# Performance work log

Hardware: AMD Instinct MI355X
Metric: run time of the kernel (lower is better)

The kernel has to match this reference:

```python
import jax, jax.numpy as jnp
import numpy as np

IN_F = 4096
OUT_F = 11008
GROUP_SIZE = 128
NUM_GROUPS = (IN_F + GROUP_SIZE - 1) // GROUP_SIZE  # 32
N_HIGH = int(OUT_F * 0.25)   # 2752
N_LOW = OUT_F - N_HIGH       # 8256
B, S = 2, 2048


def setup_inputs() -> dict:
    key = jax.random.key(0)
    ks = jax.random.split(key, 9)
    x = jax.random.normal(ks[0], (B, S, IN_F), dtype=jnp.float32)
    # INT8 symmetric codes for high-precision columns
    high_prec_weight = jax.random.randint(ks[1], (IN_F, N_HIGH), -128, 128, dtype=jnp.int32)
    # per-group, per-column scales (positive, realistic magnitude)
    high_prec_scales = jax.random.uniform(ks[2], (NUM_GROUPS, N_HIGH), jnp.float32, 1e-4, 2e-2)
    # 4-bit asymmetric codes in [0, 15]
    low_prec_weight = jax.random.randint(ks[3], (IN_F, N_LOW), 0, 16, dtype=jnp.int32)
    low_prec_scales = jax.random.uniform(ks[4], (IN_F, 1), jnp.float32, 1e-4, 2e-2)
    low_prec_scales2 = jax.random.uniform(ks[5], (1, N_LOW), jnp.float32, 0.5, 2.0)
    low_prec_zeros = jnp.round(jax.random.uniform(ks[6], (IN_F, 1), jnp.float32, 0.0, 15.0))
    # inverse column permutation restoring original order
    col_indices_inv = jax.random.permutation(ks[7], OUT_F).astype(jnp.int64)
    bias = jax.random.normal(ks[8], (OUT_F,), dtype=jnp.float32) * 0.02
    return {
        "x": x,
        "high_prec_weight": high_prec_weight,
        "high_prec_scales": high_prec_scales,
        "low_prec_weight": low_prec_weight,
        "low_prec_scales": low_prec_scales,
        "low_prec_scales2": low_prec_scales2,
        "low_prec_zeros": low_prec_zeros,
        "col_indices_inv": col_indices_inv,
        "bias": bias,
    }


def _dequantize(high_w, high_scales, low_w, low_s1, low_s2, low_z, col_inv):
    # High: group-wise symmetric INT8 dequant. K divisible by GROUP_SIZE here (no pad).
    w_high = (high_w.astype(jnp.float32)
              .reshape(NUM_GROUPS, GROUP_SIZE, N_HIGH)
              * high_scales[:, None, :]).reshape(IN_F, N_HIGH)
    # Low: SINQ dual-scale asymmetric dequant: ((q - z) * s1) * s2
    w_low = (low_w.astype(jnp.float32) - low_z) * low_s1 * low_s2
    # Reassemble original column order: W_kn [in_features, out_features]
    w = jnp.concatenate([w_high, w_low], axis=1)[:, col_inv]
    return w


def reference(x, high_prec_weight, high_prec_scales, low_prec_weight,
              low_prec_scales, low_prec_scales2, low_prec_zeros,
              col_indices_inv, bias):
    w_kn = _dequantize(high_prec_weight, high_prec_scales, low_prec_weight,
                       low_prec_scales, low_prec_scales2, low_prec_zeros,
                       col_indices_inv)
    # F.linear(x, W_original) with W_original = w_kn.T  ->  x @ w_kn
    out = jnp.einsum('bsk,kn->bsn', x, w_kn) + bias
    return out
```

## Files before the change

### kernel.cpp

```cpp
#include <hip/hip_runtime.h>
#include <hip/hip_bf16.h>

#define IN_F   4096
#define OUT_F  11008
#define NHIGH  2752
#define NLOW   8256
#define M_TOT  4096

typedef __attribute__((ext_vector_type(8))) short bf16x8;
typedef __attribute__((ext_vector_type(4))) float f32x4;
typedef __attribute__((ext_vector_type(4))) float f32x4v;

__device__ __forceinline__ short f2bf(float f) {
    union { float f; unsigned u; } v; v.f = f;
    unsigned r = (v.u + 0x7fffu + ((v.u >> 16) & 1u)) >> 16;
    return (short)(r & 0xffffu);
}

__device__ __forceinline__ void async16(const void* g, const void* l) {
    __builtin_amdgcn_global_load_lds(
        (const __attribute__((address_space(1))) unsigned int*)g,
        (__attribute__((address_space(3))) unsigned int*)l, 16, 0, 0);
}

__global__ void fwd_perm_kernel(const int* __restrict__ cinv, int* __restrict__ fwd) {
    int n = blockIdx.x * blockDim.x + threadIdx.x;
    if (n < OUT_F) fwd[cinv[n]] = n;
}

__global__ void cvt_x_kernel(const float* __restrict__ x, short* __restrict__ xb) {
    const int nv = (M_TOT * IN_F) / 8;
    for (int i = blockIdx.x * blockDim.x + threadIdx.x; i < nv;
         i += gridDim.x * blockDim.x) {
        const f32x4v* p = (const f32x4v*)(x + (long)i * 8);
        f32x4v a = __builtin_nontemporal_load(p);
        f32x4v b = __builtin_nontemporal_load(p + 1);
        bf16x8 o;
        o[0] = f2bf(a[0]); o[1] = f2bf(a[1]); o[2] = f2bf(a[2]); o[3] = f2bf(a[3]);
        o[4] = f2bf(b[0]); o[5] = f2bf(b[1]); o[6] = f2bf(b[2]); o[7] = f2bf(b[3]);
        *(bf16x8*)(xb + (long)i * 8) = o;
    }
}

__global__ void dequant_kernel(const int* __restrict__ hw, const float* __restrict__ hs,
                               const int* __restrict__ lw, const float* __restrict__ s1,
                               const float* __restrict__ s2, const float* __restrict__ zp,
                               const int* __restrict__ fwd,
                               short* __restrict__ wt) {
    __shared__ short tile[64 * 66];
    const int t  = threadIdx.x;
    const int c0 = blockIdx.x * 64;
    const int k0 = blockIdx.y * 64;
    const int cl = t & 63;
    const int w  = t >> 6;

    if (c0 < NHIGH) {
        const int ci = c0 + cl;
        #pragma unroll
        for (int i = 0; i < 16; ++i) {
            const int kl = w + 4 * i;
            const int k  = k0 + kl;
            int   q   = __builtin_nontemporal_load(&hw[(long)k * NHIGH + ci]);
            float val = (float)q * hs[(k >> 7) * NHIGH + ci];
            tile[cl * 66 + kl] = f2bf(val);
        }
    } else {
        const int ci = c0 - NHIGH + cl;
        const float s2v = s2[ci];
        #pragma unroll
        for (int i = 0; i < 16; ++i) {
            const int kl = w + 4 * i;
            const int k  = k0 + kl;
            int   q   = __builtin_nontemporal_load(&lw[(long)k * NLOW + ci]);
            float val = ((float)q - zp[k]) * s1[k] * s2v;
            tile[cl * 66 + kl] = f2bf(val);
        }
    }
    __syncthreads();
    const int oc = t >> 2;
    const int kq = (t & 3) * 16;
    bf16x8 o0, o1;
    #pragma unroll
    for (int j = 0; j < 8; ++j) {
        o0[j] = tile[oc * 66 + kq + j];
        o1[j] = tile[oc * 66 + kq + 8 + j];
    }
    const int ndst = fwd[c0 + oc];
    short* dst = wt + (long)ndst * IN_F + k0 + kq;
    *(bf16x8*)dst       = o0;
    *(bf16x8*)(dst + 8) = o1;
}

#define BM 256
#define BN 256
#define BK 64
#define KT (IN_F / BK)
#define NTIL (OUT_F / BN)
#define MTIL (M_TOT / BM)
#define NWG2 (NTIL * MTIL)

#define BAR()    __builtin_amdgcn_s_barrier()
#define LGKM0()  asm volatile("s_waitcnt lgkmcnt(0)" ::: "memory")
#define VMC(N)   asm volatile("s_waitcnt vmcnt(" #N ")" ::: "memory")

__global__ __launch_bounds__(512, 2) void gemm_kernel(
    const short* __restrict__ A,
    const short* __restrict__ Bt,
    const float* __restrict__ bias,
    float* __restrict__ C) {
    __shared__ __align__(16) short lds_s[65536];
    char* const lds = (char*)lds_s;

    const int t    = threadIdx.x;
    const int lane = t & 63;
    const int w    = t >> 6;
    const int wr   = w >> 2;
    const int wc   = w & 3;

    const int swz = (blockIdx.x % 8) * (NWG2 / 8) + blockIdx.x / 8;
    const int nb  = swz / MTIL;
    const int mb  = swz % MTIL;
    const int m0  = mb * BM;
    const int n0  = nb * BN;

    const int srow = w * 8 + (lane >> 3);
    const int scb  = ((lane & 7) ^ (lane >> 3)) * 16;
    const char* gA0 = (const char*)A  + (long)(m0 + srow) * (IN_F * 2) + scb;
    const char* gB0 = (const char*)Bt + (long)(n0 + srow) * (IN_F * 2) + scb;

    const int rl  = (lane & 15) * 128;
    const int kb0 = ((lane >> 4) * 16) ^ ((lane & 7) << 4);
    const int kb1 = kb0 ^ 64;

#define STAGE(gbase, region_off, h, ktile) do {                                  \
        const char* _g = (gbase) + (long)((h) * 128) * (IN_F * 2) + (ktile) * 128; \
        char* _l = lds + (region_off) + (h) * 16384 + w * 1024;                  \
        async16(_g,                      _l);                                    \
        async16(_g + (long)64 * (IN_F * 2), _l + 8192);                          \
    } while (0)

    f32x4 acc[8][4];
    #pragma unroll
    for (int i = 0; i < 8; ++i)
        #pragma unroll
        for (int j = 0; j < 4; ++j)
            acc[i][j] = (f32x4){0.f, 0.f, 0.f, 0.f};

    bf16x8 a[4][2], b0[2][2], b1[2][2];

#define RD_A(buf, mq) do {                                                       \
        char* _p = lds + (buf) * 65536 + wr * 16384 + (mq) * 8192 + rl;          \
        _Pragma("unroll")                                                        \
        for (int _j = 0; _j < 4; ++_j) {                                         \
            a[_j][0] = *(const bf16x8*)(_p + _j * 2048 + kb0);                   \
            a[_j][1] = *(const bf16x8*)(_p + _j * 2048 + kb1);                   \
        }                                                                        \
    } while (0)

#define RD_B(buf, nq, breg) do {                                                 \
        char* _p = lds + (buf) * 65536 + 32768 + wc * 8192 + (nq) * 4096 + rl;   \
        _Pragma("unroll")                                                        \
        for (int _n = 0; _n < 2; ++_n) {                                         \
            breg[_n][0] = *(const bf16x8*)(_p + _n * 2048 + kb0);                \
            breg[_n][1] = *(const bf16x8*)(_p + _n * 2048 + kb1);                \
        }                                                                        \
    } while (0)

#define MMA_Q(mq, nq, breg) do {                                                 \
        __builtin_amdgcn_s_setprio(1);                                           \
        _Pragma("unroll")                                                        \
        for (int _j = 0; _j < 4; ++_j)                                           \
        _Pragma("unroll")                                                        \
        for (int _n = 0; _n < 2; ++_n) {                                         \
            acc[(mq)*4+_j][(nq)*2+_n] = __builtin_amdgcn_mfma_f32_16x16x32_bf16( \
                a[_j][0], breg[_n][0], acc[(mq)*4+_j][(nq)*2+_n], 0, 0, 0);      \
            acc[(mq)*4+_j][(nq)*2+_n] = __builtin_amdgcn_mfma_f32_16x16x32_bf16( \
                a[_j][1], breg[_n][1], acc[(mq)*4+_j][(nq)*2+_n], 0, 0, 0);      \
        }                                                                        \
        __builtin_amdgcn_s_setprio(0);                                           \
    } while (0)

    STAGE(gA0, 0,     0, 0);
    STAGE(gA0, 0,     1, 0);
    STAGE(gB0, 32768, 0, 0);
    STAGE(gB0, 32768, 1, 0);
    STAGE(gA0, 65536, 0, 1);
    VMC(2);
    BAR();

    #pragma unroll 1
    for (int it = 0; it < KT / 2; ++it) {
        const int kt1 = 2 * it + 1;
        const int kt2 = (2 * it + 2 < KT) ? 2 * it + 2 : KT - 1;
        const int kt3 = (2 * it + 3 < KT) ? 2 * it + 3 : KT - 1;

        RD_A(0, 0); RD_B(0, 0, b0);
        STAGE(gA0, 65536 + 0,     1, kt1);
        BAR(); LGKM0();
        MMA_Q(0, 0, b0);
        BAR();

        RD_B(0, 1, b1);
        STAGE(gB0, 65536 + 32768, 0, kt1);
        BAR(); LGKM0();
        MMA_Q(0, 1, b1);
        BAR();

        RD_A(0, 1);
        STAGE(gB0, 65536 + 32768, 1, kt1);
        BAR(); LGKM0();
        MMA_Q(1, 1, b1);
        BAR();

        STAGE(gA0, 0,             0, kt2);
        BAR();
        MMA_Q(1, 0, b0);
        VMC(2);
        BAR();

        RD_A(1, 0); RD_B(1, 0, b0);
        STAGE(gA0, 0,             1, kt2);
        BAR(); LGKM0();
        MMA_Q(0, 0, b0);
        BAR();

        RD_B(1, 1, b1);
        STAGE(gB0, 32768,         0, kt2);
        BAR(); LGKM0();
        MMA_Q(0, 1, b1);
        BAR();

        RD_A(1, 1);
        STAGE(gB0, 32768,         1, kt2);
        BAR(); LGKM0();
        MMA_Q(1, 1, b1);
        BAR();

        STAGE(gA0, 65536,         0, kt3);
        BAR();
        MMA_Q(1, 0, b0);
        VMC(2);
        BAR();
    }

    asm volatile("s_waitcnt vmcnt(0)" ::: "memory");

    const int er = m0 + wr * 128 + (lane >> 4) * 4;
    const int ec = n0 + wc * 64 + (lane & 15);
    #pragma unroll
    for (int ni = 0; ni < 4; ++ni) {
        const float bv = bias[ec + ni * 16];
        #pragma unroll
        for (int mi = 0; mi < 8; ++mi) {
            #pragma unroll
            for (int r = 0; r < 4; ++r) {
                __builtin_nontemporal_store(
                    acc[mi][ni][r] + bv,
                    &C[(long)(er + mi * 16 + r) * OUT_F + ec + ni * 16]);
            }
        }
    }
}

extern "C" void kernel_launch(void* const* d_in, const int* in_sizes, int n_in,
                              void* d_out, int out_size, void* d_ws, size_t ws_size,
                              hipStream_t stream) {
    const float* x    = (const float*)d_in[0];
    const int*   hw   = (const int*)d_in[1];
    const float* hs   = (const float*)d_in[2];
    const int*   lw   = (const int*)d_in[3];
    const float* s1   = (const float*)d_in[4];
    const float* s2   = (const float*)d_in[5];
    const float* zp   = (const float*)d_in[6];
    const int*   cinv = (const int*)d_in[7];
    const float* bias = (const float*)d_in[8];
    float*       out  = (float*)d_out;

    short* wt  = (short*)d_ws;
    short* xb  = (short*)((char*)d_ws + (size_t)OUT_F * IN_F * 2);
    int*   fwd = (int*)((char*)d_ws + (size_t)OUT_F * IN_F * 2
                                    + (size_t)M_TOT * IN_F * 2);

    fwd_perm_kernel<<<(OUT_F + 255) / 256, 256, 0, stream>>>(cinv, fwd);
    cvt_x_kernel<<<2048, 256, 0, stream>>>(x, xb);
    dequant_kernel<<<dim3(OUT_F / 64, IN_F / 64), 256, 0, stream>>>(
        hw, hs, lw, s1, s2, zp, fwd, wt);
    gemm_kernel<<<NWG2, 512, 0, stream>>>(xb, wt, bias, out);
}
```

Measured before the change: 404.7 us.

## Deepen async prefetch pipeline, remap wave quadrants, and use grouped tile swizzle

Changes the block-to-tile mapping so that groups of four M tiles share an N tile, aiming for better L2 reuse of B. Remaps each wave's sub-tile so a quadrant is interleaved across waves rather than contiguous. Reorders the global→LDS staging so more loads stay in flight (vmcnt 8 instead of 2), adding a wait after each MMA phase. The deeper prefetch is meant to hide memory latency, at the cost of more complex ordering and a risk of LDS hazards if the wait counts are wrong.

Measured after the change: 400.3 us. Within noise of the previous version (-1.1%).

```diff
diff --git a/kernel.cpp b/kernel.cpp
--- a/kernel.cpp
+++ b/kernel.cpp
@@ -117,11 +117,13 @@
     const int wr   = w >> 2;
     const int wc   = w & 3;
 
-    const int swz = (blockIdx.x % 8) * (NWG2 / 8) + blockIdx.x / 8;
-    const int nb  = swz / MTIL;
-    const int mb  = swz % MTIL;
-    const int m0  = mb * BM;
-    const int n0  = nb * BN;
+    const int swz   = (blockIdx.x % 8) * (NWG2 / 8) + blockIdx.x / 8;
+    const int sr    = swz / (4 * NTIL);
+    const int in_sr = swz % (4 * NTIL);
+    const int nb    = in_sr / 4;
+    const int mb    = sr * 4 + (in_sr & 3);
+    const int m0    = mb * BM;
+    const int n0    = nb * BN;
 
     const int srow = w * 8 + (lane >> 3);
     const int scb  = ((lane & 7) ^ (lane >> 3)) * 16;
@@ -135,7 +137,7 @@
 #define STAGE(gbase, region_off, h, ktile) do {                                  \
         const char* _g = (gbase) + (long)((h) * 128) * (IN_F * 2) + (ktile) * 128; \
         char* _l = lds + (region_off) + (h) * 16384 + w * 1024;                  \
-        async16(_g,                      _l);                                    \
+        async16(_g,                        _l);                                  \
         async16(_g + (long)64 * (IN_F * 2), _l + 8192);                          \
     } while (0)
 
@@ -148,8 +150,8 @@
 
     bf16x8 a[4][2], b0[2][2], b1[2][2];
 
-#define RD_A(buf, mq) do {                                                       \
-        char* _p = lds + (buf) * 65536 + wr * 16384 + (mq) * 8192 + rl;          \
+#define RD_A(buf, qm) do {                                                       \
+        char* _p = lds + (buf) * 65536 + (qm) * 16384 + wr * 8192 + rl;          \
         _Pragma("unroll")                                                        \
         for (int _j = 0; _j < 4; ++_j) {                                         \
             a[_j][0] = *(const bf16x8*)(_p + _j * 2048 + kb0);                   \
@@ -157,8 +159,8 @@
         }                                                                        \
     } while (0)
 
-#define RD_B(buf, nq, breg) do {                                                 \
-        char* _p = lds + (buf) * 65536 + 32768 + wc * 8192 + (nq) * 4096 + rl;   \
+#define RD_B(buf, qn, breg) do {                                                 \
+        char* _p = lds + (buf) * 65536 + 32768 + (qn) * 16384 + wc * 4096 + rl;  \
         _Pragma("unroll")                                                        \
         for (int _n = 0; _n < 2; ++_n) {                                         \
             breg[_n][0] = *(const bf16x8*)(_p + _n * 2048 + kb0);                \
@@ -166,97 +168,91 @@
         }                                                                        \
     } while (0)
 
-#define MMA_Q(mq, nq, breg) do {                                                 \
+#define MMA_Q(qm, qn, breg) do {                                                 \
         __builtin_amdgcn_s_setprio(1);                                           \
         _Pragma("unroll")                                                        \
         for (int _j = 0; _j < 4; ++_j)                                           \
         _Pragma("unroll")                                                        \
         for (int _n = 0; _n < 2; ++_n) {                                         \
-            acc[(mq)*4+_j][(nq)*2+_n] = __builtin_amdgcn_mfma_f32_16x16x32_bf16( \
-                a[_j][0], breg[_n][0], acc[(mq)*4+_j][(nq)*2+_n], 0, 0, 0);      \
-            acc[(mq)*4+_j][(nq)*2+_n] = __builtin_amdgcn_mfma_f32_16x16x32_bf16( \
-                a[_j][1], breg[_n][1], acc[(mq)*4+_j][(nq)*2+_n], 0, 0, 0);      \
+            acc[(qm)*4+_j][(qn)*2+_n] = __builtin_amdgcn_mfma_f32_16x16x32_bf16( \
+                a[_j][0], breg[_n][0], acc[(qm)*4+_j][(qn)*2+_n], 0, 0, 0);      \
+            acc[(qm)*4+_j][(qn)*2+_n] = __builtin_amdgcn_mfma_f32_16x16x32_bf16( \
+                a[_j][1], breg[_n][1], acc[(qm)*4+_j][(qn)*2+_n], 0, 0, 0);      \
         }                                                                        \
         __builtin_amdgcn_s_setprio(0);                                           \
     } while (0)
 
-    STAGE(gA0, 0,     0, 0);
-    STAGE(gA0, 0,     1, 0);
-    STAGE(gB0, 32768, 0, 0);
-    STAGE(gB0, 32768, 1, 0);
-    STAGE(gA0, 65536, 0, 1);
-    VMC(2);
+    STAGE(gA0, 0,             0, 0);
+    STAGE(gB0, 32768,         0, 0);
+    STAGE(gB0, 32768,         1, 0);
+    STAGE(gA0, 0,             1, 0);
+    STAGE(gA0, 65536,         0, 1);
+    STAGE(gB0, 65536 + 32768, 0, 1);
+    VMC(8);
     BAR();
 
     #pragma unroll 1
     for (int it = 0; it < KT / 2; ++it) {
         const int kt1 = 2 * it + 1;
-        const int kt2 = (2 * it + 2 < KT) ? 2 * it + 2 : KT - 1;
-        const int kt3 = (2 * it + 3 < KT) ? 2 * it + 3 : KT - 1;
+        const int c2  = (2 * it + 2 < KT) ? 2 * it + 2 : KT - 1;
+        const int c3  = (2 * it + 3 < KT) ? 2 * it + 3 : KT - 1;
+        const int r2  = (c2 & 1) * 65536;
+        const int r3  = (c3 & 1) * 65536;
 
         RD_A(0, 0); RD_B(0, 0, b0);
-        STAGE(gA0, 65536 + 0,     1, kt1);
+        STAGE(gB0, 65536 + 32768, 1, kt1);
         BAR(); LGKM0();
         MMA_Q(0, 0, b0);
-        BAR();
-
+        VMC(8); BAR();
         RD_B(0, 1, b1);
-        STAGE(gB0, 65536 + 32768, 0, kt1);
+        STAGE(gA0, 65536,         1, kt1);
         BAR(); LGKM0();
         MMA_Q(0, 1, b1);
-        BAR();
-
+        VMC(8); BAR();
         RD_A(0, 1);
-        STAGE(gB0, 65536 + 32768, 1, kt1);
+        STAGE(gA0, r2,            0, c2);
         BAR(); LGKM0();
         MMA_Q(1, 1, b1);
         BAR();
-
-        STAGE(gA0, 0,             0, kt2);
+        STAGE(gB0, r2 + 32768,    0, c2);
         BAR();
         MMA_Q(1, 0, b0);
-        VMC(2);
-        BAR();
+        VMC(8); BAR();
 
         RD_A(1, 0); RD_B(1, 0, b0);
-        STAGE(gA0, 0,             1, kt2);
+        STAGE(gB0, r2 + 32768,    1, c2);
         BAR(); LGKM0();
         MMA_Q(0, 0, b0);
-        BAR();
-
+        VMC(8); BAR();
         RD_B(1, 1, b1);
-        STAGE(gB0, 32768,         0, kt2);
+        STAGE(gA0, r2,            1, c2);
         BAR(); LGKM0();
         MMA_Q(0, 1, b1);
-        BAR();
-
+        VMC(8); BAR();
         RD_A(1, 1);
-        STAGE(gB0, 32768,         1, kt2);
+        STAGE(gA0, r3,            0, c3);
         BAR(); LGKM0();
         MMA_Q(1, 1, b1);
         BAR();
-
-        STAGE(gA0, 65536,         0, kt3);
+        STAGE(gB0, r3 + 32768,    0, c3);
         BAR();
         MMA_Q(1, 0, b0);
-        VMC(2);
-        BAR();
+        VMC(8); BAR();
     }
 
     asm volatile("s_waitcnt vmcnt(0)" ::: "memory");
 
-    const int er = m0 + wr * 128 + (lane >> 4) * 4;
-    const int ec = n0 + wc * 64 + (lane & 15);
     #pragma unroll
     for (int ni = 0; ni < 4; ++ni) {
-        const float bv = bias[ec + ni * 16];
+        const int ec = n0 + (ni >> 1) * 128 + wc * 32 + (ni & 1) * 16 + (lane & 15);
+        const float bv = bias[ec];
         #pragma unroll
         for (int mi = 0; mi < 8; ++mi) {
+            const int er = m0 + (mi >> 2) * 128 + wr * 64 + (mi & 3) * 16 + (lane >> 4) * 4;
             #pragma unroll
             for (int r = 0; r < 4; ++r) {
-                __builtin_nontemporal_store(
-                    acc[mi][ni][r] + bv,
-                    &C[(long)(er + mi * 16 + r) * OUT_F + ec + ni * 16]);
+                __builtin_nontemporal_store(acc[mi][ni][r] + bv,
+                                            &C[(long)(er + r) * OUT_F + ec]);
             }
         }
     }
```

## Switch GEMM to 32x32x16 MFMA tiles and regroup tile swizzle

Applied to the files above, without the earlier changes.

Replaces the 16x16x32 bf16 MFMA inner product with 32x32x16 MFMA, changing the LDS read pattern, accumulator layout and output epilogue to match. Larger MFMA tiles reduce LDS reads per flop and the number of MFMA issues. The block-to-tile mapping is also reordered so groups of four M tiles share each N tile, aiming for better L2 reuse. It adds an extra partial lgkmcnt wait, and the new swizzled LDS addressing has to stay bank-conflict free.

Measured after the change: 434.4 us. 7.3% more time.

```diff
diff --git a/kernel.cpp b/kernel.cpp
--- a/kernel.cpp
+++ b/kernel.cpp
@@ -9,6 +9,7 @@
 
 typedef __attribute__((ext_vector_type(8))) short bf16x8;
 typedef __attribute__((ext_vector_type(4))) float f32x4;
+typedef __attribute__((ext_vector_type(16))) float f32x16;
 typedef __attribute__((ext_vector_type(4))) float f32x4v;
 
 __device__ __forceinline__ short f2bf(float f) {
@@ -101,6 +102,7 @@
 
 #define BAR()    __builtin_amdgcn_s_barrier()
 #define LGKM0()  asm volatile("s_waitcnt lgkmcnt(0)" ::: "memory")
+#define LGKM8()  asm volatile("s_waitcnt lgkmcnt(8)" ::: "memory")
 #define VMC(N)   asm volatile("s_waitcnt vmcnt(" #N ")" ::: "memory")
 
 __global__ __launch_bounds__(512, 2) void gemm_kernel(
@@ -114,69 +116,71 @@
     const int t    = threadIdx.x;
     const int lane = t & 63;
     const int w    = t >> 6;
-    const int wr   = w >> 2;
+    const int wr   = w >> 1;
+    const int wrr  = w >> 2;
     const int wc   = w & 3;
 
-    const int swz = (blockIdx.x % 8) * (NWG2 / 8) + blockIdx.x / 8;
-    const int nb  = swz / MTIL;
-    const int mb  = swz % MTIL;
-    const int m0  = mb * BM;
-    const int n0  = nb * BN;
+    const int swz   = (blockIdx.x % 8) * (NWG2 / 8) + blockIdx.x / 8;
+    const int sr    = swz / (4 * NTIL);
+    const int in_sr = swz % (4 * NTIL);
+    const int nb    = in_sr / 4;
+    const int mb    = sr * 4 + (in_sr & 3);
+    const int m0    = mb * BM;
+    const int n0    = nb * BN;
+    (void)wr;
 
     const int srow = w * 8 + (lane >> 3);
     const int scb  = ((lane & 7) ^ (lane >> 3)) * 16;
     const char* gA0 = (const char*)A  + (long)(m0 + srow) * (IN_F * 2) + scb;
     const char* gB0 = (const char*)Bt + (long)(n0 + srow) * (IN_F * 2) + scb;
 
-    const int rl  = (lane & 15) * 128;
-    const int kb0 = ((lane >> 4) * 16) ^ ((lane & 7) << 4);
-    const int kb1 = kb0 ^ 64;
+    const int rlA = (lane & 31) * 128;
+    int kb32[4];
+    #pragma unroll
+    for (int ks = 0; ks < 4; ++ks)
+        kb32[ks] = ((ks * 2 + (lane >> 5)) ^ (lane & 7)) * 16;
 
 #define STAGE(gbase, region_off, h, ktile) do {                                  \
         const char* _g = (gbase) + (long)((h) * 128) * (IN_F * 2) + (ktile) * 128; \
         char* _l = lds + (region_off) + (h) * 16384 + w * 1024;                  \
-        async16(_g,                      _l);                                    \
+        async16(_g,                        _l);                                  \
         async16(_g + (long)64 * (IN_F * 2), _l + 8192);                          \
     } while (0)
 
-    f32x4 acc[8][4];
-    #pragma unroll
-    for (int i = 0; i < 8; ++i)
-        #pragma unroll
-        for (int j = 0; j < 4; ++j)
-            acc[i][j] = (f32x4){0.f, 0.f, 0.f, 0.f};
-
-    bf16x8 a[4][2], b0[2][2], b1[2][2];
-
-#define RD_A(buf, mq) do {                                                       \
-        char* _p = lds + (buf) * 65536 + wr * 16384 + (mq) * 8192 + rl;          \
-        _Pragma("unroll")                                                        \
-        for (int _j = 0; _j < 4; ++_j) {                                         \
-            a[_j][0] = *(const bf16x8*)(_p + _j * 2048 + kb0);                   \
-            a[_j][1] = *(const bf16x8*)(_p + _j * 2048 + kb1);                   \
-        }                                                                        \
-    } while (0)
-
-#define RD_B(buf, nq, breg) do {                                                 \
-        char* _p = lds + (buf) * 65536 + 32768 + wc * 8192 + (nq) * 4096 + rl;   \
-        _Pragma("unroll")                                                        \
-        for (int _n = 0; _n < 2; ++_n) {                                         \
-            breg[_n][0] = *(const bf16x8*)(_p + _n * 2048 + kb0);                \
-            breg[_n][1] = *(const bf16x8*)(_p + _n * 2048 + kb1);                \
-        }                                                                        \
-    } while (0)
-
-#define MMA_Q(mq, nq, breg) do {                                                 \
+    f32x16 acc[4][2];
+    #pragma unroll
+    for (int i = 0; i < 4; ++i)
+        #pragma unroll
+        for (int j = 0; j < 2; ++j)
+            acc[i][j] = (f32x16){0.f,0.f,0.f,0.f,0.f,0.f,0.f,0.f,
+                                 0.f,0.f,0.f,0.f,0.f,0.f,0.f,0.f};
+
+    bf16x8 a[2][4], b0[4], b1[4];
+
+#define RD_A32(buf, mq) do {                                                     \
+        char* _p = lds + (buf) * 65536 + wrr * 16384 + (mq) * 8192 + rlA;        \
+        _Pragma("unroll")                                                        \
+        for (int _rb = 0; _rb < 2; ++_rb)                                        \
+        _Pragma("unroll")                                                        \
+        for (int _ks = 0; _ks < 4; ++_ks)                                        \
+            a[_rb][_ks] = *(const bf16x8*)(_p + _rb * 4096 + kb32[_ks]);         \
+    } while (0)
+
+#define RD_B32(buf, nq, breg) do {                                               \
+        char* _p = lds + (buf) * 65536 + 32768 + wc * 8192 + (nq) * 4096 + rlA;  \
+        _Pragma("unroll")                                                        \
+        for (int _ks = 0; _ks < 4; ++_ks)                                        \
+            breg[_ks] = *(const bf16x8*)(_p + kb32[_ks]);                        \
+    } while (0)
+
+#define MMA_Q32(mq, nq, breg) do {                                               \
         __builtin_amdgcn_s_setprio(1);                                           \
         _Pragma("unroll")                                                        \
-        for (int _j = 0; _j < 4; ++_j)                                           \
-        _Pragma("unroll")                                                        \
-        for (int _n = 0; _n < 2; ++_n) {                                         \
-            acc[(mq)*4+_j][(nq)*2+_n] = __builtin_amdgcn_mfma_f32_16x16x32_bf16( \
-                a[_j][0], breg[_n][0], acc[(mq)*4+_j][(nq)*2+_n], 0, 0, 0);      \
-            acc[(mq)*4+_j][(nq)*2+_n] = __builtin_amdgcn_mfma_f32_16x16x32_bf16( \
-                a[_j][1], breg[_n][1], acc[(mq)*4+_j][(nq)*2+_n], 0, 0, 0);      \
-        }                                                                        \
+        for (int _ks = 0; _ks < 4; ++_ks)                                        \
+        _Pragma("unroll")                                                        \
+        for (int _rb = 0; _rb < 2; ++_rb)                                        \
+            acc[(mq)*2+_rb][(nq)] = __builtin_amdgcn_mfma_f32_32x32x16_bf16(     \
+                a[_rb][_ks], breg[_ks], acc[(mq)*2+_rb][(nq)], 0, 0, 0);         \
         __builtin_amdgcn_s_setprio(0);                                           \
     } while (0)
 
@@ -194,69 +198,74 @@
         const int kt2 = (2 * it + 2 < KT) ? 2 * it + 2 : KT - 1;
         const int kt3 = (2 * it + 3 < KT) ? 2 * it + 3 : KT - 1;
 
-        RD_A(0, 0); RD_B(0, 0, b0);
+        RD_A32(0, 0); RD_B32(0, 0, b0);
         STAGE(gA0, 65536 + 0,     1, kt1);
-        BAR(); LGKM0();
-        MMA_Q(0, 0, b0);
-        BAR();
-
-        RD_B(0, 1, b1);
+        LGKM8();
+        BAR(); LGKM0();
+        MMA_Q32(0, 0, b0);
+        BAR();
+
+        RD_B32(0, 1, b1);
         STAGE(gB0, 65536 + 32768, 0, kt1);
         BAR(); LGKM0();
-        MMA_Q(0, 1, b1);
-        BAR();
-
-        RD_A(0, 1);
+        MMA_Q32(0, 1, b1);
+        BAR();
+
+        RD_A32(0, 1);
         STAGE(gB0, 65536 + 32768, 1, kt1);
         BAR(); LGKM0();
-        MMA_Q(1, 1, b1);
+        MMA_Q32(1, 1, b1);
         BAR();
 
         STAGE(gA0, 0,             0, kt2);
         BAR();
-        MMA_Q(1, 0, b0);
+        MMA_Q32(1, 0, b0);
         VMC(2);
         BAR();
 
-        RD_A(1, 0); RD_B(1, 0, b0);
+        RD_A32(1, 0); RD_B32(1, 0, b0);
         STAGE(gA0, 0,             1, kt2);
-        BAR(); LGKM0();
-        MMA_Q(0, 0, b0);
-        BAR();
-
-        RD_B(1, 1, b1);
+        LGKM8();
+        BAR(); LGKM0();
+        MMA_Q32(0, 0, b0);
+        BAR();
+
+        RD_B32(1, 1, b1);
         STAGE(gB0, 32768,         0, kt2);
         BAR(); LGKM0();
-        MMA_Q(0, 1, b1);
-        BAR();
-
-        RD_A(1, 1);
+        MMA_Q32(0, 1, b1);
+        BAR();
+
+        RD_A32(1, 1);
         STAGE(gB0, 32768,         1, kt2);
         BAR(); LGKM0();
-        MMA_Q(1, 1, b1);
+        MMA_Q32(1, 1, b1);
         BAR();
 
         STAGE(gA0, 65536,         0, kt3);
         BAR();
-        MMA_Q(1, 0, b0);
+        MMA_Q32(1, 0, b0);
         VMC(2);
         BAR();
     }
 
     asm volatile("s_waitcnt vmcnt(0)" ::: "memory");
 
-    const int er = m0 + wr * 128 + (lane >> 4) * 4;
-    const int ec = n0 + wc * 64 + (lane & 15);
-    #pragma unroll
-    for (int ni = 0; ni < 4; ++ni) {
-        const float bv = bias[ec + ni * 16];
-        #pragma unroll
-        for (int mi = 0; mi < 8; ++mi) {
+    #pragma unroll
+    for (int fn = 0; fn < 2; ++fn) {
+        const int ec = n0 + wc * 64 + fn * 32 + (lane & 31);
+        const float bv = bias[ec];
+        #pragma unroll
+        for (int fm = 0; fm < 4; ++fm) {
+            const int rbase = m0 + wrr * 128 + fm * 32 + 4 * (lane >> 5);
             #pragma unroll
-            for (int r = 0; r < 4; ++r) {
-                __builtin_nontemporal_store(
-                    acc[mi][ni][r] + bv,
-                    &C[(long)(er + mi * 16 + r) * OUT_F + ec + ni * 16]);
+            for (int g = 0; g < 4; ++g) {
+                #pragma unroll
+                for (int q = 0; q < 4; ++q) {
+                    __builtin_nontemporal_store(
+                        acc[fm][fn][g * 4 + q] + bv,
+                        &C[(long)(rbase + 8 * g + q) * OUT_F + ec]);
+                }
             }
         }
     }
```
